# Kernel optimization log

Hardware: AMD Instinct MI355X
Metric: run time of the kernel (lower is better)

## Reference

```python
import jax, jax.numpy as jnp
import numpy as np

B, L, C, H = 4, 1024, 768, 12
D = C // H  # head_ch = 64


def setup_inputs() -> dict:
    key = jax.random.key(0)
    ks = jax.random.split(key, 8)
    s = 1.0 / np.sqrt(C)
    return {
        "inputs_q": jax.random.normal(ks[0], (B, L, C), jnp.float32),
        "inputs_kv": jax.random.normal(ks[1], (B, L, C), jnp.float32),
        "Wq": jax.random.normal(ks[2], (C, H * D), jnp.float32) * s,
        "Wk": jax.random.normal(ks[3], (C, H * D), jnp.float32) * s,
        "Wv": jax.random.normal(ks[4], (C, H * D), jnp.float32) * s,
        "Wout": jax.random.normal(ks[5], (H * D, C), jnp.float32) * s,
        "W_pre": jax.random.normal(ks[6], (H, H), jnp.float32) * (1.0 / np.sqrt(H)),
        "W_post": jax.random.normal(ks[7], (H, H), jnp.float32) * (1.0 / np.sqrt(H)),
    }


def reference(inputs_q, inputs_kv, Wq, Wk, Wv, Wout, W_pre, W_post):
    # Linear projections (no bias), split into heads: b l (h d) -> b h l d
    def split_heads(x):
        b, l, _ = x.shape
        return x.reshape(b, l, H, D).transpose(0, 2, 1, 3)

    q = split_heads(inputs_q @ Wq) / jnp.sqrt(jnp.asarray(D, inputs_q.dtype))
    k = split_heads(inputs_kv @ Wk)
    v = split_heads(inputs_kv @ Wv)

    # Attention logits [b, h, l, k]
    weights = jnp.einsum('bhld,bhkd->bhlk', q, k)
    # Talking-heads: learned cross-head mixing pre-softmax
    weights = jnp.einsum('bhlk,hi->bilk', weights, W_pre)
    weights = jax.nn.softmax(weights, axis=-1)
    # Talking-heads post-softmax mixing
    weights = jnp.einsum('bhlk,hi->bilk', weights, W_post)

    scores = jnp.einsum('bhlk,bhkd->bhld', weights, v)
    scores = scores.transpose(0, 2, 1, 3).reshape(B, L, H * D)  # b l (h d)
    return scores @ Wout
```

## Files before the change

kernel.cpp:

```cpp
#include <hip/hip_runtime.h>

#define BB 4
#define LL 1024
#define CC 768
#define HH 12
#define DD 64

typedef unsigned short ushort_t;
typedef __attribute__((ext_vector_type(8))) short bf16x8;
typedef __attribute__((ext_vector_type(4))) float f32x4;
typedef __attribute__((ext_vector_type(2))) float f32x2;

__device__ inline ushort_t f2bf(float x) {
    union { float f; unsigned u; } v; v.f = x;
    unsigned r = (v.u + 0x7FFFu + ((v.u >> 16) & 1u)) >> 16;
    return (ushort_t)r;
}
__device__ inline float bf2f(ushort_t u) {
    union { unsigned u; float f; } v; v.u = ((unsigned)u) << 16;
    return v.f;
}
__device__ inline float u2f(unsigned u) {
    union { unsigned u; float f; } v; v.u = u;
    return v.f;
}

__device__ inline void stage_rows(const ushort_t* __restrict__ g, int stride,
                                  ushort_t* lds, int nbytes, int wave, int lane) {
    const int ko = (lane & 3) << 3;
    const int rsub = lane >> 2;
    for (int off = wave * 1024; off < nbytes; off += 4096) {
        int row = (off >> 6) + rsub;
        __builtin_amdgcn_global_load_lds(
            (const __attribute__((address_space(1))) void*)(g + (size_t)row * stride + ko),
            (__attribute__((address_space(3))) void*)(lds + (off >> 1)),
            16, 0, 0);
    }
}

__global__ __launch_bounds__(256) void prep(const float* __restrict__ q, const float* __restrict__ kv,
                                            const float* __restrict__ w0, const float* __restrict__ w1,
                                            const float* __restrict__ w2, const float* __restrict__ w3,
                                            ushort_t* __restrict__ qo, ushort_t* __restrict__ kvo,
                                            ushort_t* __restrict__ o0, ushort_t* __restrict__ o1,
                                            ushort_t* __restrict__ o2, ushort_t* __restrict__ o3) {
    __shared__ float t[32][33];
    const int bx = blockIdx.x;
    if (bx < 3072) {
        const float* src = bx < 1536 ? q : kv;
        ushort_t* dst = bx < 1536 ? qo : kvo;
        int bb = bx < 1536 ? bx : bx - 1536;
        size_t i = ((size_t)bb * 256 + threadIdx.x) * 8;
        float4 a = *(const float4*)(src + i);
        float4 b = *(const float4*)(src + i + 4);
        ushort_t u[8] = {f2bf(a.x), f2bf(a.y), f2bf(a.z), f2bf(a.w),
                         f2bf(b.x), f2bf(b.y), f2bf(b.z), f2bf(b.w)};
        *(uint4*)(dst + i) = *(uint4*)u;
    } else {
        int w = bx - 3072;
        int z = w / 576, rem = w % 576;
        const float* W = z == 0 ? w0 : z == 1 ? w1 : z == 2 ? w2 : w3;
        ushort_t* Wt   = z == 0 ? o0 : z == 1 ? o1 : z == 2 ? o2 : o3;
        const int c = threadIdx.x & 31, r0 = threadIdx.x >> 5;
        const int kb = (rem / 24) * 32, nb = (rem % 24) * 32;
#pragma unroll
        for (int i = 0; i < 4; ++i)
            t[r0 + 8 * i][c] = W[(size_t)(kb + r0 + 8 * i) * CC + nb + c];
        __syncthreads();
#pragma unroll
        for (int i = 0; i < 4; ++i)
            Wt[(size_t)(nb + r0 + 8 * i) * CC + kb + c] = f2bf(t[c][r0 + 8 * i]);
    }
}

__global__ __launch_bounds__(256) void proj_gemm(const ushort_t* __restrict__ Aq,
                                                 const ushort_t* __restrict__ Akv,
                                                 const ushort_t* __restrict__ Wqt,
                                                 const ushort_t* __restrict__ Wkt,
                                                 const ushort_t* __restrict__ Wvt,
                                                 ushort_t* __restrict__ Qo,
                                                 ushort_t* __restrict__ Ko,
                                                 ushort_t* __restrict__ Vto) {
    const int z = blockIdx.z;
    const ushort_t* A  = (z == 0) ? Aq : Akv;
    const ushort_t* Wt = (z == 0) ? Wqt : (z == 1 ? Wkt : Wvt);

    __shared__ __align__(16) ushort_t a_lds[128 * 32];
    __shared__ __align__(16) ushort_t b_lds[128 * 32];

    const int tid = threadIdx.x;
    const int bm = blockIdx.x * 128, bn = blockIdx.y * 128;
    const int wave = tid >> 6, lane = tid & 63;
    const int quad = lane >> 4, lq = lane & 15;
    const int wr = wave >> 1, wc = wave & 1;

    f32x4 acc[4][4] = {};

    for (int k0 = 0; k0 < CC; k0 += 32) {
        stage_rows(A + (size_t)bm * CC + k0, CC, a_lds, 8192, wave, lane);
        stage_rows(Wt + (size_t)bn * CC + k0, CC, b_lds, 8192, wave, lane);
        __syncthreads();
        bf16x8 af[4], bfr[4];
#pragma unroll
        for (int mi = 0; mi < 4; ++mi)
            af[mi] = *(bf16x8*)&a_lds[(wr * 64 + mi * 16 + lq) * 32 + quad * 8];
#pragma unroll
        for (int ni = 0; ni < 4; ++ni)
            bfr[ni] = *(bf16x8*)&b_lds[(wc * 64 + ni * 16 + lq) * 32 + quad * 8];
#pragma unroll
        for (int mi = 0; mi < 4; ++mi)
#pragma unroll
            for (int ni = 0; ni < 4; ++ni)
                acc[mi][ni] = __builtin_amdgcn_mfma_f32_16x16x32_bf16(af[mi], bfr[ni], acc[mi][ni], 0, 0, 0);
        __syncthreads();
    }

    const float scale = (z == 0) ? 0.125f : 1.0f;
#pragma unroll
    for (int mi = 0; mi < 4; ++mi)
#pragma unroll
        for (int ni = 0; ni < 4; ++ni)
#pragma unroll
            for (int r = 0; r < 4; ++r) {
                int row = bm + wr * 64 + mi * 16 + quad * 4 + r;
                int col = bn + wc * 64 + ni * 16 + lq;
                int b = row >> 10, l = row & 1023, h = col >> 6, d = col & 63;
                ushort_t v = f2bf(acc[mi][ni][r] * scale);
                if (z == 0)      Qo[((size_t)(b * HH + h) * LL + l) * DD + d] = v;
                else if (z == 1) Ko[((size_t)(b * HH + h) * LL + l) * DD + d] = v;
                else             Vto[((size_t)(b * HH + h) * DD + d) * LL + l] = v;
            }
}

__global__ __launch_bounds__(256) void qk_premix(const ushort_t* __restrict__ Q,
                                                 const ushort_t* __restrict__ K,
                                                 const float* __restrict__ Wpre,
                                                 ushort_t* __restrict__ S,
                                                 float* __restrict__ z) {
    __shared__ __align__(16) ushort_t qt[2][128 * 32];
    __shared__ __align__(16) ushort_t kt[2][64 * 32];
    __shared__ __align__(16) ushort_t T[HH * 64 * 32];

    const int tid = threadIdx.x;
    const int k0 = blockIdx.x * 32, l0 = blockIdx.y * 64, b = blockIdx.z;
    const int wave = tid >> 6, lane = tid & 63;
    const int quad = lane >> 4, lq = lane & 15;

    {
        const ushort_t* Qh = Q + ((size_t)(b * HH) * LL + l0) * DD;
        const ushort_t* Kh = K + ((size_t)(b * HH) * LL + k0) * DD;
        stage_rows(Qh,      DD, qt[0],        4096, wave, lane);
        stage_rows(Qh + 32, DD, qt[0] + 2048, 4096, wave, lane);
        stage_rows(Kh,      DD, kt[0],        2048, wave, lane);
        stage_rows(Kh + 32, DD, kt[0] + 1024, 2048, wave, lane);
    }

    for (int h = 0; h < HH; ++h) {
        const int cur = h & 1, nxt = cur ^ 1;
        __syncthreads();
        if (h + 1 < HH) {
            const ushort_t* Qh = Q + ((size_t)(b * HH + h + 1) * LL + l0) * DD;
            const ushort_t* Kh = K + ((size_t)(b * HH + h + 1) * LL + k0) * DD;
            stage_rows(Qh,      DD, qt[nxt],        4096, wave, lane);
            stage_rows(Qh + 32, DD, qt[nxt] + 2048, 4096, wave, lane);
            stage_rows(Kh,      DD, kt[nxt],        2048, wave, lane);
            stage_rows(Kh + 32, DD, kt[nxt] + 1024, 2048, wave, lane);
        }
        f32x4 acc[2] = {};
#pragma unroll
        for (int ks = 0; ks < 2; ++ks) {
            bf16x8 af = *(bf16x8*)&qt[cur][(ks * 64 + wave * 16 + lq) * 32 + quad * 8];
#pragma unroll
            for (int nt = 0; nt < 2; ++nt) {
                bf16x8 bf = *(bf16x8*)&kt[cur][(ks * 32 + nt * 16 + lq) * 32 + quad * 8];
                acc[nt] = __builtin_amdgcn_mfma_f32_16x16x32_bf16(af, bf, acc[nt], 0, 0, 0);
            }
        }
#pragma unroll
        for (int nt = 0; nt < 2; ++nt)
#pragma unroll
            for (int r = 0; r < 4; ++r) {
                int l = wave * 16 + quad * 4 + r;
                T[(h * 64 + l) * 32 + nt * 16 + lq] = f2bf(acc[nt][r]);
            }
    }
    __syncthreads();

    const int l = tid >> 2, k8 = (tid & 3) * 8;
    f32x2 pa[HH][4];
#pragma unroll
    for (int i = 0; i < HH; ++i) { pa[i][0] = 0.f; pa[i][1] = 0.f; pa[i][2] = 0.f; pa[i][3] = 0.f; }
#pragma unroll
    for (int h = 0; h < HH; ++h) {
        uint4 raw = *(uint4*)&T[(h * 64 + l) * 32 + k8];
        f32x2 v[4];
        v[0].x = u2f(raw.x << 16); v[0].y = u2f(raw.x & 0xFFFF0000u);
        v[1].x = u2f(raw.y << 16); v[1].y = u2f(raw.y & 0xFFFF0000u);
        v[2].x = u2f(raw.z << 16); v[2].y = u2f(raw.z & 0xFFFF0000u);
        v[3].x = u2f(raw.w << 16); v[3].y = u2f(raw.w & 0xFFFF0000u);
#pragma unroll
        for (int i = 0; i < HH; ++i) {
            float w = Wpre[h * HH + i];
            pa[i][0] += v[0] * w; pa[i][1] += v[1] * w;
            pa[i][2] += v[2] * w; pa[i][3] += v[3] * w;
        }
    }

    float zs[HH];
#pragma unroll
    for (int i = 0; i < HH; ++i) {
        ushort_t u[8];
        float e = 0.f;
#pragma unroll
        for (int j = 0; j < 4; ++j) {
            u[2 * j]     = f2bf(pa[i][j].x);
            u[2 * j + 1] = f2bf(pa[i][j].y);
            e += __expf(bf2f(u[2 * j])) + __expf(bf2f(u[2 * j + 1]));
        }
        zs[i] = e;
        *(uint4*)&S[((size_t)(b * HH + i) * LL + l0 + l) * LL + k0 + k8] = *(uint4*)u;
    }
#pragma unroll
    for (int i = 0; i < HH; ++i) {
        float zr = zs[i];
        zr += __shfl_xor(zr, 1);
        zr += __shfl_xor(zr, 2);
        if ((tid & 3) == 0)
            atomicAdd(&z[(size_t)(b * HH + i) * LL + l0 + l], zr);
    }
}

__global__ __launch_bounds__(256) void pv_fused(const ushort_t* __restrict__ S,
                                                const ushort_t* __restrict__ Vt,
                                                const float* __restrict__ z,
                                                const float* __restrict__ Wpost,
                                                ushort_t* __restrict__ att) {
    __shared__ __align__(16) ushort_t sp[2][HH * 16 * 32];
    __shared__ __align__(16) ushort_t vt[2][HH * 64 * 32];
    __shared__ __align__(16) ushort_t pp[HH * 16 * 40];

    const int tid = threadIdx.x;
    const int l0 = blockIdx.x * 16, b = blockIdx.y;
    const int wave = tid >> 6, lane = tid & 63;
    const int quad = lane >> 4, lq = lane & 15;
    const int co = (tid & 3) * 8, r0 = tid >> 2;
    const int la = tid >> 4, k2 = (tid & 15) * 2;

    float invr[HH];
#pragma unroll
    for (int h = 0; h < HH; ++h)
        invr[h] = 1.0f / z[(size_t)(b * HH + h) * LL + l0 + la];

#pragma unroll
    for (int s = 0; s < 3; ++s) {
        int row = r0 + 64 * s, i = row >> 4, l = row & 15;
        __builtin_amdgcn_global_load_lds(
            (const __attribute__((address_space(1))) void*)(S + ((size_t)(b * HH + i) * LL + l0 + l) * LL + co),
            (__attribute__((address_space(3))) void*)(sp[0] + row * 32 + co), 16, 0, 0);
    }
#pragma unroll
    for (int s = 0; s < 12; ++s) {
        int row = r0 + 64 * s, i = row >> 6, d = row & 63;
        __builtin_amdgcn_global_load_lds(
            (const __attribute__((address_space(1))) void*)(Vt + ((size_t)(b * HH + i) * DD + d) * LL + co),
            (__attribute__((address_space(3))) void*)(vt[0] + row * 32 + co), 16, 0, 0);
    }

    f32x4 acco[HH] = {};

    for (int n = 0; n < 32; ++n) {
        const int cur = n & 1, nxt = cur ^ 1;
        __syncthreads();

        f32x2 pacc[HH];
#pragma unroll
        for (int i = 0; i < HH; ++i) pacc[i] = 0.f;
#pragma unroll
        for (int h = 0; h < HH; ++h) {
            unsigned raw = *(unsigned*)&sp[cur][h * 512 + la * 32 + k2];
            f32x2 e;
            e.x = __expf(u2f(raw << 16)) * invr[h];
            e.y = __expf(u2f(raw & 0xFFFF0000u)) * invr[h];
#pragma unroll
            for (int i = 0; i < HH; ++i)
                pacc[i] += e * Wpost[h * HH + i];
        }
#pragma unroll
        for (int i = 0; i < HH; ++i) {
            ushort_t u[2] = {f2bf(pacc[i].x), f2bf(pacc[i].y)};
            *(unsigned*)&pp[i * 640 + la * 40 + k2] = *(unsigned*)u;
        }
        __syncthreads();

        if (n + 1 < 32) {
            int k0n = (n + 1) * 32;
#pragma unroll
            for (int s = 0; s < 3; ++s) {
                int row = r0 + 64 * s, i = row >> 4, l = row & 15;
                __builtin_amdgcn_global_load_lds(
                    (const __attribute__((address_space(1))) void*)(S + ((size_t)(b * HH + i) * LL + l0 + l) * LL + k0n + co),
                    (__attribute__((address_space(3))) void*)(sp[nxt] + row * 32 + co), 16, 0, 0);
            }
#pragma unroll
            for (int s = 0; s < 12; ++s) {
                int row = r0 + 64 * s, i = row >> 6, d = row & 63;
                __builtin_amdgcn_global_load_lds(
                    (const __attribute__((address_space(1))) void*)(Vt + ((size_t)(b * HH + i) * DD + d) * LL + k0n + co),
                    (__attribute__((address_space(3))) void*)(vt[nxt] + row * 32 + co), 16, 0, 0);
            }
        }

#pragma unroll
        for (int i = 0; i < HH; ++i) {
            bf16x8 a  = *(bf16x8*)&pp[i * 640 + lq * 40 + quad * 8];
            bf16x8 bv = *(bf16x8*)&vt[cur][i * 2048 + (wave * 16 + lq) * 32 + quad * 8];
            acco[i] = __builtin_amdgcn_mfma_f32_16x16x32_bf16(a, bv, acco[i], 0, 0, 0);
        }
    }

#pragma unroll
    for (int i = 0; i < HH; ++i)
#pragma unroll
        for (int r = 0; r < 4; ++r)
            att[((size_t)(b * LL) + l0 + quad * 4 + r) * CC + i * DD + wave * 16 + lq] = f2bf(acco[i][r]);
}

__global__ __launch_bounds__(256) void out_gemm(const ushort_t* __restrict__ A,
                                                const ushort_t* __restrict__ Wt,
                                                float* __restrict__ out) {
    __shared__ __align__(16) ushort_t a_lds[128 * 32];
    __shared__ __align__(16) ushort_t b_lds[64 * 32];

    const int tid = threadIdx.x;
    const int bm = blockIdx.x * 128, bn = blockIdx.y * 64;
    const int wave = tid >> 6, lane = tid & 63;
    const int quad = lane >> 4, lq = lane & 15;
    const int wr = wave >> 1, wc = wave & 1;

    f32x4 acc[4][2] = {};

    for (int k0 = 0; k0 < CC; k0 += 32) {
        stage_rows(A + (size_t)bm * CC + k0, CC, a_lds, 8192, wave, lane);
        stage_rows(Wt + (size_t)bn * CC + k0, CC, b_lds, 4096, wave, lane);
        __syncthreads();
        bf16x8 af[4], bfr[2];
#pragma unroll
        for (int mi = 0; mi < 4; ++mi)
            af[mi] = *(bf16x8*)&a_lds[(wr * 64 + mi * 16 + lq) * 32 + quad * 8];
#pragma unroll
        for (int ni = 0; ni < 2; ++ni)
            bfr[ni] = *(bf16x8*)&b_lds[(wc * 32 + ni * 16 + lq) * 32 + quad * 8];
#pragma unroll
        for (int mi = 0; mi < 4; ++mi)
#pragma unroll
            for (int ni = 0; ni < 2; ++ni)
                acc[mi][ni] = __builtin_amdgcn_mfma_f32_16x16x32_bf16(af[mi], bfr[ni], acc[mi][ni], 0, 0, 0);
        __syncthreads();
    }

#pragma unroll
    for (int mi = 0; mi < 4; ++mi)
#pragma unroll
        for (int ni = 0; ni < 2; ++ni)
#pragma unroll
            for (int r = 0; r < 4; ++r) {
                int row = bm + wr * 64 + mi * 16 + quad * 4 + r;
                int col = bn + wc * 32 + ni * 16 + lq;
                out[(size_t)row * CC + col] = acc[mi][ni][r];
            }
}

extern "C" void kernel_launch(void* const* d_in, const int* in_sizes, int n_in,
                              void* d_out, int out_size, void* d_ws, size_t ws_size,
                              hipStream_t stream) {
    const float* inputs_q  = (const float*)d_in[0];
    const float* inputs_kv = (const float*)d_in[1];
    const float* Wq   = (const float*)d_in[2];
    const float* Wk   = (const float*)d_in[3];
    const float* Wv   = (const float*)d_in[4];
    const float* Wout = (const float*)d_in[5];
    const float* Wpre  = (const float*)d_in[6];
    const float* Wpost = (const float*)d_in[7];
    float* out = (float*)d_out;

    const size_t nS   = (size_t)BB * HH * LL * LL;
    const size_t nQKV = (size_t)BB * HH * LL * DD;
    const size_t nW   = (size_t)CC * CC;

    ushort_t* Sb   = (ushort_t*)d_ws;
    ushort_t* Qb   = Sb + nS;
    ushort_t* Kb   = Qb + nQKV;
    ushort_t* Vtb  = Kb + nQKV;
    ushort_t* attb = Vtb + nQKV;
    ushort_t* inq  = attb + nQKV;
    ushort_t* inkv = inq + nQKV;
    ushort_t* Wqt  = inkv + nQKV;
    ushort_t* Wkt  = Wqt + nW;
    ushort_t* Wvt  = Wkt + nW;
    ushort_t* Wot  = Wvt + nW;
    float*    zbuf = (float*)(Wot + nW);

    dim3 blk(256);

    hipMemsetAsync(zbuf, 0, (size_t)BB * HH * LL * sizeof(float), stream);
    prep<<<dim3(5376), blk, 0, stream>>>(inputs_q, inputs_kv, Wq, Wk, Wv, Wout,
                                         inq, inkv, Wqt, Wkt, Wvt, Wot);
    proj_gemm<<<dim3(32, 6, 3), blk, 0, stream>>>(inq, inkv, Wqt, Wkt, Wvt, Qb, Kb, Vtb);
    qk_premix<<<dim3(32, 16, BB), blk, 0, stream>>>(Qb, Kb, Wpre, Sb, zbuf);
    pv_fused<<<dim3(64, BB), blk, 0, stream>>>(Sb, Vtb, zbuf, Wpost, attb);
    out_gemm<<<dim3(32, 12), blk, 0, stream>>>(attb, Wot, out);
}
```

Baseline: 284.9 us.

## Split PV kernel over key halves and sum partials in output GEMM

The PV kernel now splits the key dimension into two halves across a new grid axis, doubling the block count from 256 to 512 to fill more CUs. Each half writes fp32 partial attention outputs, which the output GEMM sums and converts to bf16 while staging its A tile. V tiles are now read straight from global memory instead of being staged into LDS, and the softmax inverse normalisers move into shared memory to free registers. The cost is extra fp32 partial-buffer traffic, a fatter A load in the output GEMM, and uncoalesced direct V loads.

```diff
diff --git a/kernel.cpp b/kernel.cpp
--- a/kernel.cpp
+++ b/kernel.cpp
@@ -234,41 +234,37 @@
                                                 const ushort_t* __restrict__ Vt,
                                                 const float* __restrict__ z,
                                                 const float* __restrict__ Wpost,
-                                                ushort_t* __restrict__ att) {
+                                                float* __restrict__ attF) {
     __shared__ __align__(16) ushort_t sp[2][HH * 16 * 32];
-    __shared__ __align__(16) ushort_t vt[2][HH * 64 * 32];
     __shared__ __align__(16) ushort_t pp[HH * 16 * 40];
+    __shared__ float zinv[HH * 16];
 
     const int tid = threadIdx.x;
-    const int l0 = blockIdx.x * 16, b = blockIdx.y;
+    const int l0 = blockIdx.x * 16;
+    const int ks = blockIdx.y;
+    const int b  = blockIdx.z;
     const int wave = tid >> 6, lane = tid & 63;
     const int quad = lane >> 4, lq = lane & 15;
-    const int co = (tid & 3) * 8, r0 = tid >> 2;
-    const int la = tid >> 4, k2 = (tid & 15) * 2;
-
-    float invr[HH];
-#pragma unroll
-    for (int h = 0; h < HH; ++h)
-        invr[h] = 1.0f / z[(size_t)(b * HH + h) * LL + l0 + la];
-
+    const int srow = tid >> 2, sco = (tid & 3) * 8;
+    const int la = tid >> 4, kp = (tid & 15) * 2;
+
+    if (tid < HH * 16) {
+        int h = tid >> 4, l = tid & 15;
+        zinv[tid] = 1.0f / z[(size_t)(b * HH + h) * LL + l0 + l];
+    }
+
+    const int kbase = ks * 512;
 #pragma unroll
     for (int s = 0; s < 3; ++s) {
-        int row = r0 + 64 * s, i = row >> 4, l = row & 15;
+        int row = srow + 64 * s, i = row >> 4, l = row & 15;
         __builtin_amdgcn_global_load_lds(
-            (const __attribute__((address_space(1))) void*)(S + ((size_t)(b * HH + i) * LL + l0 + l) * LL + co),
-            (__attribute__((address_space(3))) void*)(sp[0] + row * 32 + co), 16, 0, 0);
-    }
-#pragma unroll
-    for (int s = 0; s < 12; ++s) {
-        int row = r0 + 64 * s, i = row >> 6, d = row & 63;
-        __builtin_amdgcn_global_load_lds(
-            (const __attribute__((address_space(1))) void*)(Vt + ((size_t)(b * HH + i) * DD + d) * LL + co),
-            (__attribute__((address_space(3))) void*)(vt[0] + row * 32 + co), 16, 0, 0);
+            (const __attribute__((address_space(1))) void*)(S + ((size_t)(b * HH + i) * LL + l0 + l) * LL + kbase + sco),
+            (__attribute__((address_space(3))) void*)(sp[0] + row * 32 + sco), 16, 0, 0);
     }
 
     f32x4 acco[HH] = {};
 
-    for (int n = 0; n < 32; ++n) {
+    for (int n = 0; n < 16; ++n) {
         const int cur = n & 1, nxt = cur ^ 1;
         __syncthreads();
 
@@ -277,10 +273,11 @@
         for (int i = 0; i < HH; ++i) pacc[i] = 0.f;
 #pragma unroll
         for (int h = 0; h < HH; ++h) {
-            unsigned raw = *(unsigned*)&sp[cur][h * 512 + la * 32 + k2];
+            unsigned raw = *(unsigned*)&sp[cur][h * 512 + la * 32 + kp];
+            float iv = zinv[h * 16 + la];
             f32x2 e;
-            e.x = __expf(u2f(raw << 16)) * invr[h];
-            e.y = __expf(u2f(raw & 0xFFFF0000u)) * invr[h];
+            e.x = __expf(u2f(raw << 16)) * iv;
+            e.y = __expf(u2f(raw & 0xFFFF0000u)) * iv;
 #pragma unroll
             for (int i = 0; i < HH; ++i)
                 pacc[i] += e * Wpost[h * HH + i];
@@ -288,47 +285,43 @@
 #pragma unroll
         for (int i = 0; i < HH; ++i) {
             ushort_t u[2] = {f2bf(pacc[i].x), f2bf(pacc[i].y)};
-            *(unsigned*)&pp[i * 640 + la * 40 + k2] = *(unsigned*)u;
-        }
-        __syncthreads();
-
-        if (n + 1 < 32) {
-            int k0n = (n + 1) * 32;
+            *(unsigned*)&pp[i * 640 + la * 40 + kp] = *(unsigned*)u;
+        }
+        __syncthreads();
+
+        if (n + 1 < 16) {
+            int ka = kbase + (n + 1) * 32;
 #pragma unroll
             for (int s = 0; s < 3; ++s) {
-                int row = r0 + 64 * s, i = row >> 4, l = row & 15;
+                int row = srow + 64 * s, i = row >> 4, l = row & 15;
                 __builtin_amdgcn_global_load_lds(
-                    (const __attribute__((address_space(1))) void*)(S + ((size_t)(b * HH + i) * LL + l0 + l) * LL + k0n + co),
-                    (__attribute__((address_space(3))) void*)(sp[nxt] + row * 32 + co), 16, 0, 0);
+                    (const __attribute__((address_space(1))) void*)(S + ((size_t)(b * HH + i) * LL + l0 + l) * LL + ka + sco),
+                    (__attribute__((address_space(3))) void*)(sp[nxt] + row * 32 + sco), 16, 0, 0);
             }
-#pragma unroll
-            for (int s = 0; s < 12; ++s) {
-                int row = r0 + 64 * s, i = row >> 6, d = row & 63;
-                __builtin_amdgcn_global_load_lds(
-                    (const __attribute__((address_space(1))) void*)(Vt + ((size_t)(b * HH + i) * DD + d) * LL + k0n + co),
-                    (__attribute__((address_space(3))) void*)(vt[nxt] + row * 32 + co), 16, 0, 0);
-            }
-        }
-
+        }
+
+        const int ka = kbase + n * 32;
 #pragma unroll
         for (int i = 0; i < HH; ++i) {
             bf16x8 a  = *(bf16x8*)&pp[i * 640 + lq * 40 + quad * 8];
-            bf16x8 bv = *(bf16x8*)&vt[cur][i * 2048 + (wave * 16 + lq) * 32 + quad * 8];
+            bf16x8 bv = *(const bf16x8*)&Vt[((size_t)(b * HH + i) * DD + wave * 16 + lq) * LL + ka + quad * 8];
             acco[i] = __builtin_amdgcn_mfma_f32_16x16x32_bf16(a, bv, acco[i], 0, 0, 0);
         }
     }
 
+    float* ab = attF + (size_t)ks * ((size_t)BB * LL * CC);
 #pragma unroll
     for (int i = 0; i < HH; ++i)
 #pragma unroll
         for (int r = 0; r < 4; ++r)
-            att[((size_t)(b * LL) + l0 + quad * 4 + r) * CC + i * DD + wave * 16 + lq] = f2bf(acco[i][r]);
-}
-
-__global__ __launch_bounds__(256) void out_gemm(const ushort_t* __restrict__ A,
+            ab[((size_t)(b * LL) + l0 + quad * 4 + r) * CC + i * DD + wave * 16 + lq] = acco[i][r];
+}
+
+__global__ __launch_bounds__(256) void out_gemm(const float* __restrict__ A0,
+                                                const float* __restrict__ A1,
                                                 const ushort_t* __restrict__ Wt,
                                                 float* __restrict__ out) {
-    __shared__ __align__(16) ushort_t a_lds[128 * 32];
+    __shared__ __align__(16) float a_lds[128 * 36];
     __shared__ __align__(16) ushort_t b_lds[64 * 32];
 
     const int tid = threadIdx.x;
@@ -340,13 +333,28 @@
     f32x4 acc[4][2] = {};
 
     for (int k0 = 0; k0 < CC; k0 += 32) {
-        stage_rows(A + (size_t)bm * CC + k0, CC, a_lds, 8192, wave, lane);
+#pragma unroll
+        for (int j = 0; j < 4; ++j) {
+            int idx = tid + j * 256;
+            int r = idx >> 3, c4 = (idx & 7) * 4;
+            float4 x = *(const float4*)&A0[(size_t)(bm + r) * CC + k0 + c4];
+            float4 y = *(const float4*)&A1[(size_t)(bm + r) * CC + k0 + c4];
+            x.x += y.x; x.y += y.y; x.z += y.z; x.w += y.w;
+            *(float4*)&a_lds[r * 36 + c4] = x;
+        }
         stage_rows(Wt + (size_t)bn * CC + k0, CC, b_lds, 4096, wave, lane);
         __syncthreads();
+
         bf16x8 af[4], bfr[2];
 #pragma unroll
-        for (int mi = 0; mi < 4; ++mi)
-            af[mi] = *(bf16x8*)&a_lds[(wr * 64 + mi * 16 + lq) * 32 + quad * 8];
+        for (int mi = 0; mi < 4; ++mi) {
+            int row = wr * 64 + mi * 16 + lq;
+            float4 x = *(float4*)&a_lds[row * 36 + quad * 8];
+            float4 y = *(float4*)&a_lds[row * 36 + quad * 8 + 4];
+            ushort_t uu[8] = {f2bf(x.x), f2bf(x.y), f2bf(x.z), f2bf(x.w),
+                              f2bf(y.x), f2bf(y.y), f2bf(y.z), f2bf(y.w)};
+            af[mi] = *(bf16x8*)uu;
+        }
 #pragma unroll
         for (int ni = 0; ni < 2; ++ni)
             bfr[ni] = *(bf16x8*)&b_lds[(wc * 32 + ni * 16 + lq) * 32 + quad * 8];
@@ -386,19 +394,20 @@
     const size_t nS   = (size_t)BB * HH * LL * LL;
     const size_t nQKV = (size_t)BB * HH * LL * DD;
     const size_t nW   = (size_t)CC * CC;
+    const size_t nAtt = (size_t)BB * LL * CC;
 
     ushort_t* Sb   = (ushort_t*)d_ws;
     ushort_t* Qb   = Sb + nS;
     ushort_t* Kb   = Qb + nQKV;
     ushort_t* Vtb  = Kb + nQKV;
-    ushort_t* attb = Vtb + nQKV;
-    ushort_t* inq  = attb + nQKV;
+    ushort_t* inq  = Vtb + nQKV;
     ushort_t* inkv = inq + nQKV;
     ushort_t* Wqt  = inkv + nQKV;
     ushort_t* Wkt  = Wqt + nW;
     ushort_t* Wvt  = Wkt + nW;
     ushort_t* Wot  = Wvt + nW;
-    float*    zbuf = (float*)(Wot + nW);
+    float*    attF = (float*)(Wot + nW);
+    float*    zbuf = attF + 2 * nAtt;
 
     dim3 blk(256);
 
@@ -407,6 +416,6 @@
                                          inq, inkv, Wqt, Wkt, Wvt, Wot);
     proj_gemm<<<dim3(32, 6, 3), blk, 0, stream>>>(inq, inkv, Wqt, Wkt, Wvt, Qb, Kb, Vtb);
     qk_premix<<<dim3(32, 16, BB), blk, 0, stream>>>(Qb, Kb, Wpre, Sb, zbuf);
-    pv_fused<<<dim3(64, BB), blk, 0, stream>>>(Sb, Vtb, zbuf, Wpost, attb);
-    out_gemm<<<dim3(32, 12), blk, 0, stream>>>(attb, Wot, out);
-}
+    pv_fused<<<dim3(64, 2, BB), blk, 0, stream>>>(Sb, Vtb, zbuf, Wpost, attF);
+    out_gemm<<<dim3(32, 12), blk, 0, stream>>>(attF, attF + nAtt, Wot, out);
+}
```

After: 309.9 us. 8.8% more time.
